# Optimization experiments

Hardware: AMD Instinct MI355X
Metric: run time of the kernel (lower is better)

The kernel has to match this reference:

```python
import jax, jax.numpy as jnp
import numpy as np

BATCH, SEQ, CHANNELS, KSIZE = 4, 4096, 2048, 4


def setup_inputs() -> dict:
    key = jax.random.key(0)
    kx, kw = jax.random.split(key)
    x = jax.random.normal(kx, (BATCH, SEQ, CHANNELS), dtype=jnp.float32)
    # flax param init: normal(stddev=0.02), shape (kernel_size, channels)
    kernel = jax.random.normal(kw, (KSIZE, CHANNELS), dtype=jnp.float32) * 0.02
    return {"x": x, "kernel": kernel}


def reference(x, kernel):
    # Causal depthwise short conv: y[:, t] = silu(sum_j kernel[j] * x[:, t - j])
    # (the scan's window * kernel[::-1] unrolls to exactly this), with zero
    # left-padding of K-1 steps standing in for cache=None -> zeros.
    B, T, C = x.shape
    K = kernel.shape[0]
    kf = kernel.astype(x.dtype)
    cache = jnp.zeros((B, K - 1, C), dtype=x.dtype)
    xp = jnp.concatenate([cache, x], axis=1)  # [B, T+K-1, C]
    # Small fixed loop over kernel taps (K=4), fully parallel over time.
    y = kf[0][None, None, :] * xp[:, K - 1 : K - 1 + T, :]
    for j in range(1, K):
        y = y + kf[j][None, None, :] * xp[:, K - 1 - j : K - 1 - j + T, :]
    y = jax.nn.silu(y)
    # next_cache after the scan = last K-1 inputs of the padded stream
    next_cache = xp[:, T:, :]  # [B, K-1, C]
    return y, next_cache
```

## Files before the change

### kernel.cpp

```cpp
#include <hip/hip_runtime.h>
#include <math.h>


#define B_   4
#define T_   4096
#define C_   2048
#define K_   4
#define C4_  (C_ / 4)
#define TT_  16

typedef float nat_float4 __attribute__((ext_vector_type(4)));

__device__ __forceinline__ float silu_f(float v) {
    return v * __frcp_rn(1.f + __expf(-v));
}

__device__ __forceinline__ void store_nt(float4* p, const float4& v) {
    nat_float4 nv = { v.x, v.y, v.z, v.w };
    __builtin_nontemporal_store(nv, reinterpret_cast<nat_float4*>(p));
}

__global__ __launch_bounds__(C4_, 8) void dwconv_silu_kernel(
    const float4* __restrict__ x,
    const float4* __restrict__ kern,
    float4* __restrict__ y)
{
    const int c4 = threadIdx.x;
    const int b  = blockIdx.y;
    const int t0 = blockIdx.x * TT_;

    const float4 k0 = kern[0 * C4_ + c4];
    const float4 k1 = kern[1 * C4_ + c4];
    const float4 k2 = kern[2 * C4_ + c4];
    const float4 k3 = kern[3 * C4_ + c4];

    const float4* xb = x + (size_t)b * T_ * C4_ + c4;
    float4*       yb = y + (size_t)b * T_ * C4_ + c4;

    float4 xm1, xm2, xm3;
    if (t0 == 0) {
        xm1 = make_float4(0.f, 0.f, 0.f, 0.f);
        xm2 = xm1;
        xm3 = xm1;
    } else {
        xm1 = xb[(size_t)(t0 - 1) * C4_];
        xm2 = xb[(size_t)(t0 - 2) * C4_];
        xm3 = xb[(size_t)(t0 - 3) * C4_];
    }

#define CONV1(r, a, w1, w2, w3)                                              \
    r.x = fmaf(k0.x, a.x, fmaf(k1.x, w1.x, fmaf(k2.x, w2.x, k3.x * w3.x)));  \
    r.y = fmaf(k0.y, a.y, fmaf(k1.y, w1.y, fmaf(k2.y, w2.y, k3.y * w3.y)));  \
    r.z = fmaf(k0.z, a.z, fmaf(k1.z, w1.z, fmaf(k2.z, w2.z, k3.z * w3.z)));  \
    r.w = fmaf(k0.w, a.w, fmaf(k1.w, w1.w, fmaf(k2.w, w2.w, k3.w * w3.w)));  \
    r.x = silu_f(r.x); r.y = silu_f(r.y); r.z = silu_f(r.z); r.w = silu_f(r.w);

    #pragma unroll
    for (int i = 0; i < TT_; i += 4) {
        const float4 a0 = xb[(size_t)(t0 + i + 0) * C4_];
        const float4 a1 = xb[(size_t)(t0 + i + 1) * C4_];
        const float4 a2 = xb[(size_t)(t0 + i + 2) * C4_];
        const float4 a3 = xb[(size_t)(t0 + i + 3) * C4_];

        float4 r0, r1, r2, r3;
        CONV1(r0, a0, xm1, xm2, xm3)
        CONV1(r1, a1, a0,  xm1, xm2)
        CONV1(r2, a2, a1,  a0,  xm1)
        CONV1(r3, a3, a2,  a1,  a0)

        store_nt(&yb[(size_t)(t0 + i + 0) * C4_], r0);
        store_nt(&yb[(size_t)(t0 + i + 1) * C4_], r1);
        store_nt(&yb[(size_t)(t0 + i + 2) * C4_], r2);
        store_nt(&yb[(size_t)(t0 + i + 3) * C4_], r3);

        xm3 = a1;
        xm2 = a2;
        xm1 = a3;
    }
#undef CONV1
}

__global__ __launch_bounds__(256) void cache_copy_kernel(
    const float4* __restrict__ x, float4* __restrict__ cache)
{
    const int i = blockIdx.x * blockDim.x + threadIdx.x;
    if (i >= B_ * (K_ - 1) * C4_) return;
    const int b  = i / ((K_ - 1) * C4_);
    const int rc = i % ((K_ - 1) * C4_);
    const int t  = T_ - (K_ - 1) + rc / C4_;
    const int c4 = rc % C4_;
    cache[i] = x[((size_t)b * T_ + t) * C4_ + c4];
}

extern "C" void kernel_launch(void* const* d_in, const int* in_sizes, int n_in,
                              void* d_out, int out_size, void* d_ws, size_t ws_size,
                              hipStream_t stream)
{
    const float4* x    = (const float4*)d_in[0];
    const float4* kern = (const float4*)d_in[1];
    float*        out  = (float*)d_out;

    float4* y     = (float4*)out;
    float4* cache = (float4*)(out + (size_t)B_ * T_ * C_);

    dim3 grid(T_ / TT_, B_);
    dim3 block(C4_);
    dwconv_silu_kernel<<<grid, block, 0, stream>>>(x, kern, y);

    const int cache_elems4 = B_ * (K_ - 1) * C4_;
    cache_copy_kernel<<<(cache_elems4 + 255) / 256, 256, 0, stream>>>(x, cache);
}
```

Before: 238.5 us.

## Fuse cache copy into conv kernel and software-prefetch next input rows

Removes the separate cache-copy kernel launch by having the last time-block write the final three input rows into the cache output. The main loop now loads the next four rows before computing the current ones, so load latency can overlap with arithmetic. It also swaps the correctly rounded reciprocal for the hardware rcp builtin and lowers the launch-bounds occupancy hint from 8 to 4, which gives more registers per thread for the extra in-flight loads. The cost is higher register pressure and slightly less precise SiLU.

```diff
diff --git a/kernel.cpp b/kernel.cpp
--- a/kernel.cpp
+++ b/kernel.cpp
@@ -12,7 +12,7 @@
 typedef float nat_float4 __attribute__((ext_vector_type(4)));
 
 __device__ __forceinline__ float silu_f(float v) {
-    return v * __frcp_rn(1.f + __expf(-v));
+    return v * __builtin_amdgcn_rcpf(1.f + __expf(-v));
 }
 
 __device__ __forceinline__ void store_nt(float4* p, const float4& v) {
@@ -20,10 +20,11 @@
     __builtin_nontemporal_store(nv, reinterpret_cast<nat_float4*>(p));
 }
 
-__global__ __launch_bounds__(C4_, 8) void dwconv_silu_kernel(
+__global__ __launch_bounds__(C4_, 4) void dwconv_silu_kernel(
     const float4* __restrict__ x,
     const float4* __restrict__ kern,
-    float4* __restrict__ y)
+    float4* __restrict__ y,
+    float4* __restrict__ cache)
 {
     const int c4 = threadIdx.x;
     const int b  = blockIdx.y;
@@ -34,8 +35,8 @@
     const float4 k2 = kern[2 * C4_ + c4];
     const float4 k3 = kern[3 * C4_ + c4];
 
-    const float4* xb = x + (size_t)b * T_ * C4_ + c4;
-    float4*       yb = y + (size_t)b * T_ * C4_ + c4;
+    const float4* xr = x + ((size_t)b * T_ + t0) * C4_ + c4;
+    float4*       yr = y + ((size_t)b * T_ + t0) * C4_ + c4;
 
     float4 xm1, xm2, xm3;
     if (t0 == 0) {
@@ -43,10 +44,16 @@
         xm2 = xm1;
         xm3 = xm1;
     } else {
-        xm1 = xb[(size_t)(t0 - 1) * C4_];
-        xm2 = xb[(size_t)(t0 - 2) * C4_];
-        xm3 = xb[(size_t)(t0 - 3) * C4_];
+        xm1 = xr[-1 * C4_];
+        xm2 = xr[-2 * C4_];
+        xm3 = xr[-3 * C4_];
     }
+
+    float4 a0 = xr[0 * C4_];
+    float4 a1 = xr[1 * C4_];
+    float4 a2 = xr[2 * C4_];
+    float4 a3 = xr[3 * C4_];
+    xr += 4 * C4_;
 
 #define CONV1(r, a, w1, w2, w3)                                              \
     r.x = fmaf(k0.x, a.x, fmaf(k1.x, w1.x, fmaf(k2.x, w2.x, k3.x * w3.x)));  \
@@ -57,10 +64,14 @@
 
     #pragma unroll
     for (int i = 0; i < TT_; i += 4) {
-        const float4 a0 = xb[(size_t)(t0 + i + 0) * C4_];
-        const float4 a1 = xb[(size_t)(t0 + i + 1) * C4_];
-        const float4 a2 = xb[(size_t)(t0 + i + 2) * C4_];
-        const float4 a3 = xb[(size_t)(t0 + i + 3) * C4_];
+        float4 n0, n1, n2, n3;
+        if (i + 4 < TT_) {
+            n0 = xr[0 * C4_];
+            n1 = xr[1 * C4_];
+            n2 = xr[2 * C4_];
+            n3 = xr[3 * C4_];
+            xr += 4 * C4_;
+        }
 
         float4 r0, r1, r2, r3;
         CONV1(r0, a0, xm1, xm2, xm3)
@@ -68,28 +79,28 @@
         CONV1(r2, a2, a1,  a0,  xm1)
         CONV1(r3, a3, a2,  a1,  a0)
 
-        store_nt(&yb[(size_t)(t0 + i + 0) * C4_], r0);
-        store_nt(&yb[(size_t)(t0 + i + 1) * C4_], r1);
-        store_nt(&yb[(size_t)(t0 + i + 2) * C4_], r2);
-        store_nt(&yb[(size_t)(t0 + i + 3) * C4_], r3);
+        store_nt(&yr[0 * C4_], r0);
+        store_nt(&yr[1 * C4_], r1);
+        store_nt(&yr[2 * C4_], r2);
+        store_nt(&yr[3 * C4_], r3);
+        yr += 4 * C4_;
 
         xm3 = a1;
         xm2 = a2;
         xm1 = a3;
+
+        if (i + 4 < TT_) {
+            a0 = n0; a1 = n1; a2 = n2; a3 = n3;
+        }
     }
 #undef CONV1
-}
 
-__global__ __launch_bounds__(256) void cache_copy_kernel(
-    const float4* __restrict__ x, float4* __restrict__ cache)
-{
-    const int i = blockIdx.x * blockDim.x + threadIdx.x;
-    if (i >= B_ * (K_ - 1) * C4_) return;
-    const int b  = i / ((K_ - 1) * C4_);
-    const int rc = i % ((K_ - 1) * C4_);
-    const int t  = T_ - (K_ - 1) + rc / C4_;
-    const int c4 = rc % C4_;
-    cache[i] = x[((size_t)b * T_ + t) * C4_ + c4];
+    if (t0 == T_ - TT_) {
+        float4* cb = cache + (size_t)b * (K_ - 1) * C4_ + c4;
+        cb[0 * C4_] = xm3;
+        cb[1 * C4_] = xm2;
+        cb[2 * C4_] = xm1;
+    }
 }
 
 extern "C" void kernel_launch(void* const* d_in, const int* in_sizes, int n_in,
@@ -105,8 +116,5 @@
 
     dim3 grid(T_ / TT_, B_);
     dim3 block(C4_);
-    dwconv_silu_kernel<<<grid, block, 0, stream>>>(x, kern, y);
-
-    const int cache_elems4 = B_ * (K_ - 1) * C4_;
-    cache_copy_kernel<<<(cache_elems4 + 255) / 256, 256, 0, stream>>>(x, cache);
+    dwconv_silu_kernel<<<grid, block, 0, stream>>>(x, kern, y, cache);
 }
```

Result: no change. 235.0 us (-1.5%).
